# Kernel tuning notes

Measured on AMD Instinct MI355X. Metric: run time of the kernel, lower is better.

Reference implementation:

```python
import jax, jax.numpy as jnp
import numpy as np

D, H, DK, DF = 512, 8, 64, 2048  # dim, heads, head_dim, forward_dim
EPS = 1e-5


def _layernorm(x, g, b):
    mu = jnp.mean(x, axis=-1, keepdims=True)
    var = jnp.mean(jnp.square(x - mu), axis=-1, keepdims=True)
    return (x - mu) * jax.lax.rsqrt(var + EPS) * g + b


def setup_inputs() -> dict:
    key = jax.random.key(0)
    ks = jax.random.split(key, 16)
    B, S = 2, 2048
    s_in = 1.0 / np.sqrt(D)
    s_ff = 1.0 / np.sqrt(DF)
    s_cat = 1.0 / np.sqrt(H * DK)
    return {
        "x": jax.random.normal(ks[0], (B, S, D), jnp.float32),
        # per-head Q/K/V projections stacked over heads: [H, D, DK]
        "Wq": jax.random.uniform(ks[1], (H, D, DK), jnp.float32, -s_in, s_in),
        "bq": jax.random.uniform(ks[2], (H, DK), jnp.float32, -s_in, s_in),
        "Wk": jax.random.uniform(ks[3], (H, D, DK), jnp.float32, -s_in, s_in),
        "bk": jax.random.uniform(ks[4], (H, DK), jnp.float32, -s_in, s_in),
        "Wv": jax.random.uniform(ks[5], (H, D, DK), jnp.float32, -s_in, s_in),
        "bv": jax.random.uniform(ks[6], (H, DK), jnp.float32, -s_in, s_in),
        "Wo": jax.random.uniform(ks[7], (H * DK, D), jnp.float32, -s_cat, s_cat),
        "bo": jax.random.uniform(ks[8], (D,), jnp.float32, -s_cat, s_cat),
        "ln1_g": jnp.ones((D,), jnp.float32),
        "ln1_b": jnp.zeros((D,), jnp.float32),
        "W1": jax.random.uniform(ks[9], (D, DF), jnp.float32, -s_in, s_in),
        "b1": jax.random.uniform(ks[10], (DF,), jnp.float32, -s_in, s_in),
        "W2": jax.random.uniform(ks[11], (DF, D), jnp.float32, -s_ff, s_ff),
        "b2": jax.random.uniform(ks[12], (D,), jnp.float32, -s_ff, s_ff),
        "ln2_g": jnp.ones((D,), jnp.float32),
        "ln2_b": jnp.zeros((D,), jnp.float32),
    }


def reference(x, Wq, bq, Wk, bk, Wv, bv, Wo, bo, ln1_g, ln1_b, W1, b1, W2, b2, ln2_g, ln2_b):
    # Per-head projections, batched over heads: [B,H,S,DK]
    q = jnp.einsum('bsd,hdk->bhsk', x, Wq) + bq[None, :, None, :]
    k = jnp.einsum('bsd,hdk->bhsk', x, Wk) + bk[None, :, None, :]
    v = jnp.einsum('bsd,hdk->bhsk', x, Wv) + bv[None, :, None, :]
    scale = 1.0 / np.sqrt(DK)
    scores = jnp.einsum('bhsk,bhtk->bhst', q, k) * scale  # [B,H,S,S]
    attn = jax.nn.softmax(scores, axis=-1)
    o = jnp.einsum('bhst,bhtk->bhsk', attn, v)  # [B,H,S,DK]
    # concat heads (head order matches torch cat over ModuleList)
    B, _, S, _ = o.shape
    o = o.transpose(0, 2, 1, 3).reshape(B, S, H * DK)
    attn_out = o @ Wo + bo
    # Residual 1 (dropout = identity in eval): LN(x + sublayer(x))
    h = _layernorm(x + attn_out, ln1_g, ln1_b)
    # FeedForward + Residual 2
    ff = jax.nn.relu(h @ W1 + b1) @ W2 + b2
    return _layernorm(h + ff, ln2_g, ln2_b)
```

## Files before the change

### kernel.cpp

```cpp
#include <hip/hip_runtime.h>


#define Dm   512
#define Hh   8
#define DKk  64
#define DFf  2048
#define Bb   2
#define Ss   2048
#define Nn   4096

typedef __attribute__((ext_vector_type(8))) short short8;
typedef __attribute__((ext_vector_type(4))) float f32x4;
typedef __attribute__((ext_vector_type(4))) short short4v;

__device__ inline float bf2f(short s) {
    unsigned u = ((unsigned)(unsigned short)s) << 16;
    float f; __builtin_memcpy(&f, &u, 4); return f;
}
__device__ inline short f2bf(float f) {
    unsigned u; __builtin_memcpy(&u, &f, 4);
    u = (u + 0x7fff + ((u >> 16) & 1)) >> 16;
    return (short)u;
}
__device__ inline short cvt_elem(const void* p, long i, int f32flag) {
    if (f32flag) return f2bf(((const float*)p)[i]);
    return ((const short*)p)[i];
}
__device__ inline void gload_lds16(const short* g, short* l) {
    __builtin_amdgcn_global_load_lds(
        (const __attribute__((address_space(1))) unsigned int*)g,
        (__attribute__((address_space(3))) unsigned int*)l, 16, 0, 0);
}

__global__ __launch_bounds__(256) void detect_kernel(const void* x, int* flag)
{
    __shared__ int cnt;
    if (threadIdx.x == 0) cnt = 0;
    __syncthreads();
    const float* xf = (const float*)x;
    int ok = 0;
    for (int i = threadIdx.x; i < 1024; i += 256) {
        float a = fabsf(xf[i]);
        if (a > 1e-8f && a < 1e4f) ok++;
    }
    atomicAdd(&cnt, ok);
    __syncthreads();
    if (threadIdx.x == 0) *flag = (cnt >= 512) ? 1 : 0;
}

__global__ __launch_bounds__(256) void convert_kernel(
    const int* __restrict__ flag, const void* __restrict__ x, short* __restrict__ xb,
    const void* bq, const void* bk, const void* bv, const void* bo,
    const void* b1, const void* b2, const void* g1, const void* be1,
    const void* g2, const void* be2, short* __restrict__ smalls)
{
    int f = *flag;
    int blk = blockIdx.x;
    if (blk < 512) {
        long base = (long)blk * 4096;
        for (int i = threadIdx.x; i < 4096; i += 256)
            xb[base + i] = cvt_elem(x, base + i, f);
    } else {
        const void* srcs[10] = {bq, bk, bv, bo, b1, b2, g1, be1, g2, be2};
        const int   sz[10]   = {512, 512, 512, 512, 2048, 512, 512, 512, 512, 512};
        int off = 0;
        for (int j = 0; j < 10; ++j) {
            for (int i = threadIdx.x; i < sz[j]; i += 256)
                smalls[off + i] = cvt_elem(srcs[j], i, f);
            off += sz[j];
        }
    }
}

__global__ __launch_bounds__(256) void transpose_kernel(
    const int* __restrict__ flag,
    const void* Wq, const void* Wk, const void* Wv,
    const void* Wo, const void* W1, const void* W2,
    short* __restrict__ WqkvT,
    short* __restrict__ WoT, short* __restrict__ W1T, short* __restrict__ W2T)
{
    __shared__ short tile[64][65];
    int f = *flag;
    int blk = blockIdx.x;
    const void* src; short* dst; long srcoff = 0; long dstoff = 0; int R, C, tr, tc;
    if (blk < 192) {
        int m = blk >> 6; int r = blk & 63; int h = r >> 3; int t = r & 7;
        src = (m == 0) ? Wq : (m == 1) ? Wk : Wv;
        dst = WqkvT + (long)m * 512 * 512;
        srcoff = (long)h * 512 * 64; dstoff = (long)h * 64 * 512;
        R = 512; C = 64; tr = t; tc = 0;
    } else if (blk < 256) {
        int r = blk - 192; src = Wo; dst = WoT; R = 512; C = 512; tr = r >> 3; tc = r & 7;
    } else if (blk < 512) {
        int r = blk - 256; src = W1; dst = W1T; R = 512; C = 2048; tr = r >> 5; tc = r & 31;
    } else {
        int r = blk - 512; src = W2; dst = W2T; R = 2048; C = 512; tr = r >> 3; tc = r & 7;
    }
    int r0 = tr * 64, c0 = tc * 64;
    for (int i = threadIdx.x; i < 4096; i += 256) {
        int rr = i >> 6, cc = i & 63;
        tile[rr][cc] = cvt_elem(src, srcoff + (long)(r0 + rr) * C + c0 + cc, f);
    }
    __syncthreads();
    for (int i = threadIdx.x; i < 4096; i += 256) {
        int cc = i >> 6, rr = i & 63;
        dst[dstoff + (long)(c0 + cc) * R + r0 + rr] = tile[rr][cc];
    }
}

#define MODE_F32       1
#define MODE_RELU_BF16 2
#define MODE_QKV       4

__global__ __launch_bounds__(256) void gemm_kernel(
    const short* __restrict__ A, const short* __restrict__ Bt,
    const short* __restrict__ bias, void* __restrict__ outp,
    void* __restrict__ out2, void* __restrict__ out3,
    int K, int Ncols, int mode, int Ktile)
{
    __shared__ short As[128 * 32];
    __shared__ short Bs[128 * 32];
    const int t    = threadIdx.x;
    const int lane = t & 63;
    const int wave = t >> 6;
    const int quad = lane >> 4;
    const int l15  = lane & 15;
    const int wm = wave >> 1, wn = wave & 1;
    const int row0 = blockIdx.x * 128;
    const int col0 = blockIdx.y * 128;
    const int kbase = blockIdx.z * Ktile;

    const int srow = t >> 2;
    const int sch  = (t & 3) ^ ((t >> 3) & 3);
    const long ga0 = (long)(row0 + srow) * K + sch * 8 + kbase;
    const long ga1 = (long)(row0 + srow + 64) * K + sch * 8 + kbase;
    const long gb0 = (long)(col0 + srow) * K + sch * 8 + kbase;
    const long gb1 = (long)(col0 + srow + 64) * K + sch * 8 + kbase;
    short* la0 = As + t * 8;
    short* la1 = As + (t + 256) * 8;
    short* lb0 = Bs + t * 8;
    short* lb1 = Bs + (t + 256) * 8;

    f32x4 acc[4][4];
#pragma unroll
    for (int i = 0; i < 4; ++i)
#pragma unroll
        for (int j = 0; j < 4; ++j) acc[i][j] = (f32x4){0.f, 0.f, 0.f, 0.f};

    int aoff[4], boff[4];
#pragma unroll
    for (int mt = 0; mt < 4; ++mt) {
        int rowa = wm * 64 + mt * 16 + l15;
        aoff[mt] = rowa * 32 + (quad ^ ((rowa >> 1) & 3)) * 8;
        int rowb = wn * 64 + mt * 16 + l15;
        boff[mt] = rowb * 32 + (quad ^ ((rowb >> 1) & 3)) * 8;
    }

    for (int k0 = 0; k0 < Ktile; k0 += 32) {
        __syncthreads();
        gload_lds16(A  + ga0 + k0, la0);
        gload_lds16(A  + ga1 + k0, la1);
        gload_lds16(Bt + gb0 + k0, lb0);
        gload_lds16(Bt + gb1 + k0, lb1);
        asm volatile("s_waitcnt vmcnt(0)" ::: "memory");
        __syncthreads();
        short8 af[4], bf[4];
#pragma unroll
        for (int mt = 0; mt < 4; ++mt) af[mt] = *(const short8*)(As + aoff[mt]);
#pragma unroll
        for (int nt = 0; nt < 4; ++nt) bf[nt] = *(const short8*)(Bs + boff[nt]);
#pragma unroll
        for (int mt = 0; mt < 4; ++mt)
#pragma unroll
            for (int nt = 0; nt < 4; ++nt)
                acc[mt][nt] = __builtin_amdgcn_mfma_f32_16x16x32_bf16(
                    af[mt], bf[nt], acc[mt][nt], 0, 0, 0);
    }

    const int wrow0 = row0 + wm * 64;
    const int wcol0 = col0 + wn * 64;
    if (mode == MODE_QKV) {
        int m = wcol0 >> 9;
        if (m < 2) {
            short* out = (short*)(m == 0 ? outp : out2);
#pragma unroll
            for (int nt = 0; nt < 4; ++nt) {
                int col = wcol0 + nt * 16 + l15;
                float bb = bf2f(bias[col]);
                int cl = col & 511;
#pragma unroll
                for (int mt = 0; mt < 4; ++mt)
#pragma unroll
                    for (int r = 0; r < 4; ++r) {
                        int row = wrow0 + mt * 16 + quad * 4 + r;
                        out[(long)row * 512 + cl] = f2bf(acc[mt][nt][r] + bb);
                    }
            }
        } else {
            short* out = (short*)out3;
#pragma unroll
            for (int nt = 0; nt < 4; ++nt) {
                int col = wcol0 + nt * 16 + l15;
                float bb = bf2f(bias[col]);
                int cl = col - 1024;
                int h = cl >> 6, kk = cl & 63;
#pragma unroll
                for (int mt = 0; mt < 4; ++mt)
#pragma unroll
                    for (int r = 0; r < 4; ++r) {
                        int row = wrow0 + mt * 16 + quad * 4 + r;
                        int b = row >> 11, s = row & 2047;
                        out[((long)(b * Hh + h) * DKk + kk) * Ss + s] =
                            f2bf(acc[mt][nt][r] + bb);
                    }
            }
        }
    } else if (mode == MODE_F32) {
        float* out = (float*)outp + (long)blockIdx.z * Nn * Ncols;
        int zb = (blockIdx.z == 0);
#pragma unroll
        for (int nt = 0; nt < 4; ++nt) {
            int col = wcol0 + nt * 16 + l15;
            float bb = zb ? bf2f(bias[col]) : 0.f;
#pragma unroll
            for (int mt = 0; mt < 4; ++mt)
#pragma unroll
                for (int r = 0; r < 4; ++r) {
                    int row = wrow0 + mt * 16 + quad * 4 + r;
                    out[(long)row * Ncols + col] = acc[mt][nt][r] + bb;
                }
        }
    } else {
        short* out = (short*)outp;
#pragma unroll
        for (int nt = 0; nt < 4; ++nt) {
            int col = wcol0 + nt * 16 + l15;
            float bb = bf2f(bias[col]);
#pragma unroll
            for (int mt = 0; mt < 4; ++mt)
#pragma unroll
                for (int r = 0; r < 4; ++r) {
                    int row = wrow0 + mt * 16 + quad * 4 + r;
                    out[(long)row * Ncols + col] = f2bf(fmaxf(acc[mt][nt][r] + bb, 0.f));
                }
        }
    }
}

__global__ __launch_bounds__(256) void attn_kernel(
    const short* __restrict__ Q, const short* __restrict__ Kt,
    const short* __restrict__ Vt, float* __restrict__ po, float* __restrict__ ls)
{
    __shared__ __align__(16) short Ks[2][64 * 64];
    __shared__ __align__(16) short Vs[2][64 * 64];
    __shared__ __align__(16) short pbuf[4][32 * 72];
    const int lane = threadIdx.x & 63;
    const int wave = threadIdx.x >> 6;
    const int quad = lane >> 4;
    const int l15  = lane & 15;
    const int qt = blockIdx.x, bh = blockIdx.y, ks = blockIdx.z;
    const int b = bh >> 3, h = bh & 7;
    const int qrow = b * Ss + qt * 128 + wave * 32;

    short8 aq[2][2];
#pragma unroll
    for (int qh = 0; qh < 2; ++qh)
#pragma unroll
        for (int kk = 0; kk < 2; ++kk)
            aq[qh][kk] = *(const short8*)(Q + (long)(qrow + qh * 16 + l15) * Dm
                                          + h * DKk + kk * 32 + quad * 8);

    f32x4 o[2][4];
    float lsum[2][4];
#pragma unroll
    for (int qh = 0; qh < 2; ++qh) {
#pragma unroll
        for (int nt = 0; nt < 4; ++nt) o[qh][nt] = (f32x4){0.f, 0.f, 0.f, 0.f};
#pragma unroll
        for (int r = 0; r < 4; ++r) lsum[qh][r] = 0.f;
    }

    const short* Kg = Kt + (long)b * Ss * Dm + h * DKk;
    const short* Vg = Vt + (long)bh * DKk * Ss;
    short* pb = pbuf[wave];
    const int t00 = ks * 512;

    const int ri = lane >> 3;
    const int ct = (lane & 7) ^ ri;
    const int ldsrow0 = wave * 16;

    auto stage = [&](int buf, int tkv) {
#pragma unroll
        for (int p = 0; p < 2; ++p) {
            int r = ldsrow0 + p * 8 + ri;
            gload_lds16(Kg + (long)(tkv + r) * Dm + ct * 8,
                        &Ks[buf][(ldsrow0 + p * 8) * 64] + lane * 8);
        }
#pragma unroll
        for (int p = 0; p < 2; ++p) {
            int r = ldsrow0 + p * 8 + ri;
            gload_lds16(Vg + (long)r * Ss + tkv + ct * 8,
                        &Vs[buf][(ldsrow0 + p * 8) * 64] + lane * 8);
        }
    };

    stage(0, t00);
    int cur = 0;
    for (int it = 0; it < 8; ++it) {
        asm volatile("s_waitcnt vmcnt(0)" ::: "memory");
        __syncthreads();
        if (it < 7) stage(cur ^ 1, t00 + (it + 1) * 64);

        f32x4 s[2][4];
#pragma unroll
        for (int j = 0; j < 4; ++j) {
            short8 kf0 = *(const short8*)&Ks[cur][(j * 16 + l15) * 64
                                                  + ((quad) ^ (l15 & 7)) * 8];
            short8 kf1 = *(const short8*)&Ks[cur][(j * 16 + l15) * 64
                                                  + ((4 + quad) ^ (l15 & 7)) * 8];
#pragma unroll
            for (int qh = 0; qh < 2; ++qh) {
                f32x4 sj = (f32x4){0.f, 0.f, 0.f, 0.f};
                sj = __builtin_amdgcn_mfma_f32_16x16x32_bf16(aq[qh][0], kf0, sj, 0, 0, 0);
                sj = __builtin_amdgcn_mfma_f32_16x16x32_bf16(aq[qh][1], kf1, sj, 0, 0, 0);
                s[qh][j] = sj;
            }
        }
#pragma unroll
        for (int qh = 0; qh < 2; ++qh)
#pragma unroll
            for (int j = 0; j < 4; ++j)
#pragma unroll
                for (int r = 0; r < 4; ++r) {
                    float p = __expf(fminf(s[qh][j][r] * 0.125f, 20.f));
                    lsum[qh][r] += p;
                    pb[(qh * 16 + quad * 4 + r) * 72 + j * 16 + l15] = f2bf(p);
                }
        asm volatile("s_waitcnt lgkmcnt(0)" ::: "memory");
#pragma unroll
        for (int c = 0; c < 2; ++c) {
            short8 ap[2];
#pragma unroll
            for (int qh = 0; qh < 2; ++qh)
                ap[qh] = *(const short8*)(pb + (qh * 16 + l15) * 72 + c * 32 + quad * 8);
#pragma unroll
            for (int nt = 0; nt < 4; ++nt) {
                short8 vf = *(const short8*)&Vs[cur][(nt * 16 + l15) * 64
                                                     + ((c * 4 + quad) ^ (l15 & 7)) * 8];
#pragma unroll
                for (int qh = 0; qh < 2; ++qh)
                    o[qh][nt] = __builtin_amdgcn_mfma_f32_16x16x32_bf16(
                        ap[qh], vf, o[qh][nt], 0, 0, 0);
            }
        }
        asm volatile("" ::: "memory");
        cur ^= 1;
    }

#pragma unroll
    for (int qh = 0; qh < 2; ++qh)
#pragma unroll
        for (int r = 0; r < 4; ++r) {
            float v = lsum[qh][r];
            v += __shfl_xor(v, 1);
            v += __shfl_xor(v, 2);
            v += __shfl_xor(v, 4);
            v += __shfl_xor(v, 8);
            lsum[qh][r] = v;
        }
    float* pob = po + ((((long)bh * 16 + qt) * 4 + ks) * 128) * 64;
#pragma unroll
    for (int qh = 0; qh < 2; ++qh)
#pragma unroll
        for (int nt = 0; nt < 4; ++nt)
#pragma unroll
            for (int r = 0; r < 4; ++r)
                pob[(wave * 32 + qh * 16 + quad * 4 + r) * 64 + nt * 16 + l15] =
                    o[qh][nt][r];
    if (l15 == 0) {
        long lbase = (((long)bh * 16 + qt) * 4 + ks) * 128 + wave * 32;
#pragma unroll
        for (int qh = 0; qh < 2; ++qh)
#pragma unroll
            for (int r = 0; r < 4; ++r)
                ls[lbase + qh * 16 + quad * 4 + r] = lsum[qh][r];
    }
}

__global__ __launch_bounds__(256) void combine_kernel(
    const float* __restrict__ po, const float* __restrict__ ls,
    short* __restrict__ O)
{
    const int qt = blockIdx.x, bh = blockIdx.y;
    const int b = bh >> 3, h = bh & 7;
    const long base = ((long)bh * 16 + qt) * 4;
    const int tid = threadIdx.x;
    const int qloc = tid >> 4;
    const int dk0 = (tid & 15) * 4;
#pragma unroll
    for (int q0 = 0; q0 < 8; ++q0) {
        int q = q0 * 16 + qloc;
        f32x4 s = (f32x4){0.f, 0.f, 0.f, 0.f};
        float L = 0.f;
#pragma unroll
        for (int ksp = 0; ksp < 4; ++ksp) {
            s += *(const f32x4*)(po + ((base + ksp) * 128 + q) * 64 + dk0);
            L += ls[(base + ksp) * 128 + q];
        }
        float inv = 1.f / L;
        short4v ov;
#pragma unroll
        for (int i = 0; i < 4; ++i) ov[i] = f2bf(s[i] * inv);
        *(short4v*)(O + (long)(b * Ss + qt * 128 + q) * Dm + h * DKk + dk0) = ov;
    }
}

__global__ __launch_bounds__(256) void ln_kernel(
    const float* __restrict__ v0, const float* __restrict__ v1,
    const float* __restrict__ v2, const float* __restrict__ v3,
    const short* __restrict__ res,
    const short* __restrict__ g, const short* __restrict__ bt,
    void* __restrict__ out, const int* __restrict__ flagp)
{
    const int row = blockIdx.x, tid = threadIdx.x;
    const long base = (long)row * Dm;
    const long i0 = base + tid, i1 = base + 256 + tid;
    float x0 = v0[i0] + bf2f(res[i0]);
    float x1 = v0[i1] + bf2f(res[i1]);
    if (v1) { x0 += v1[i0]; x1 += v1[i1]; }
    if (v2) { x0 += v2[i0]; x1 += v2[i1]; }
    if (v3) { x0 += v3[i0]; x1 += v3[i1]; }

    __shared__ float red[8];
    const int wv = tid >> 6, ln = tid & 63;
    float s = x0 + x1;
#pragma unroll
    for (int mk = 1; mk < 64; mk <<= 1) s += __shfl_xor(s, mk);
    if (!ln) red[wv] = s;
    __syncthreads();
    float mean = (red[0] + red[1] + red[2] + red[3]) * (1.f / 512.f);
    float d0 = x0 - mean, d1 = x1 - mean;
    float q = d0 * d0 + d1 * d1;
#pragma unroll
    for (int mk = 1; mk < 64; mk <<= 1) q += __shfl_xor(q, mk);
    if (!ln) red[4 + wv] = q;
    __syncthreads();
    float rs = rsqrtf((red[4] + red[5] + red[6] + red[7]) * (1.f / 512.f) + 1e-5f);
    float y0 = d0 * rs * bf2f(g[tid])       + bf2f(bt[tid]);
    float y1 = d1 * rs * bf2f(g[256 + tid]) + bf2f(bt[256 + tid]);
    int f32out = flagp ? *flagp : 0;
    if (f32out) {
        float* o = (float*)out;
        o[i0] = y0; o[i1] = y1;
    } else {
        short* o = (short*)out;
        o[i0] = f2bf(y0); o[i1] = f2bf(y1);
    }
}

extern "C" void kernel_launch(void* const* d_in, const int* in_sizes, int n_in,
                              void* d_out, int out_size, void* d_ws, size_t ws_size,
                              hipStream_t stream)
{
    (void)in_sizes; (void)n_in; (void)out_size; (void)ws_size;
    const void* x   = d_in[0];
    const void* Wq  = d_in[1];  const void* bq  = d_in[2];
    const void* Wk  = d_in[3];  const void* bk  = d_in[4];
    const void* Wv  = d_in[5];  const void* bv  = d_in[6];
    const void* Wo  = d_in[7];  const void* bo  = d_in[8];
    const void* g1  = d_in[9];  const void* be1 = d_in[10];
    const void* W1  = d_in[11]; const void* b1  = d_in[12];
    const void* W2  = d_in[13]; const void* b2  = d_in[14];
    const void* g2  = d_in[15]; const void* be2 = d_in[16];

    char* ws = (char*)d_ws;
    size_t off = 0;
    auto alloc = [&](size_t bytes) -> void* {
        void* p = ws + off; off += (bytes + 255) & ~(size_t)255; return p;
    };
    short* WqkvT = (short*)alloc((size_t)3 * Dm * Dm * 2);
    short* WoT   = (short*)alloc((size_t)Dm * Dm * 2);
    short* W1T   = (short*)alloc((size_t)DFf * Dm * 2);
    short* W2T   = (short*)alloc((size_t)Dm * DFf * 2);
    short* xb    = (short*)alloc((size_t)Nn * Dm * 2);
    short* sm    = (short*)alloc((size_t)6656 * 2);
    int*   flag  = (int*)  alloc(256);
    char*  regA  = (char*)alloc((size_t)Nn * DFf * 2);
    short* Qb    = (short*)(regA);
    short* Kb    = (short*)(regA + (size_t)Nn * Dm * 2);
    short* Vt    = (short*)(regA + (size_t)Nn * Dm * 4);
    short* Ob    = (short*)(regA + (size_t)Nn * Dm * 6);
    short* u     = (short*)(regA);
    float* wo_p  = (float*)alloc((size_t)2 * Nn * Dm * 4);
    char*  regC  = (char*)alloc((size_t)16 * 16 * 4 * 128 * 64 * 4
                                + (size_t)16 * 16 * 4 * 128 * 4);
    float* po    = (float*)regC;
    float* lsb   = (float*)(regC + (size_t)16 * 16 * 4 * 128 * 64 * 4);
    float* f2p   = (float*)regC;
    short* h_bf  = (short*)alloc((size_t)Nn * Dm * 2);

    detect_kernel<<<1, 256, 0, stream>>>(x, flag);
    convert_kernel<<<513, 256, 0, stream>>>(flag, x, xb, bq, bk, bv, bo,
                                            b1, b2, g1, be1, g2, be2, sm);
    transpose_kernel<<<768, 256, 0, stream>>>(flag, Wq, Wk, Wv, Wo, W1, W2,
                                              WqkvT, WoT, W1T, W2T);
    gemm_kernel<<<dim3(Nn / 128, 1536 / 128, 1), 256, 0, stream>>>(
        xb, WqkvT, sm + 0, Qb, Kb, Vt, Dm, 1536, MODE_QKV, Dm);
    attn_kernel<<<dim3(Ss / 128, Bb * Hh, 4), 256, 0, stream>>>(Qb, Kb, Vt, po, lsb);
    combine_kernel<<<dim3(Ss / 128, Bb * Hh), 256, 0, stream>>>(po, lsb, Ob);
    gemm_kernel<<<dim3(Nn / 128, Dm / 128, 2), 256, 0, stream>>>(
        Ob, WoT, sm + 1536, wo_p, nullptr, nullptr, Dm, Dm, MODE_F32, Dm / 2);
    ln_kernel<<<Nn, 256, 0, stream>>>(wo_p, wo_p + (long)Nn * Dm, nullptr, nullptr,
                                      xb, sm + 4608, sm + 5120, h_bf, nullptr);
    gemm_kernel<<<dim3(Nn / 128, DFf / 128, 1), 256, 0, stream>>>(
        h_bf, W1T, sm + 2048, u, nullptr, nullptr, Dm, DFf, MODE_RELU_BF16, Dm);
    gemm_kernel<<<dim3(Nn / 128, Dm / 128, 4), 256, 0, stream>>>(
        u, W2T, sm + 4096, f2p, nullptr, nullptr, DFf, Dm, MODE_F32, DFf / 4);
    ln_kernel<<<Nn, 256, 0, stream>>>(f2p, f2p + (long)Nn * Dm, f2p + (long)2 * Nn * Dm,
                                      f2p + (long)3 * Nn * Dm,
                                      h_bf, sm + 5632, sm + 6144, d_out, flag);
}
```

Before: 239.3 us.

## Fuse prep kernels, double-buffer GEMM with BK=64, store attention partials in bf16

Merges the detect, convert and transpose kernels into one prep kernel. Each block now recomputes the fp32 check inline from 16 samples instead of reading a flag. The GEMM moves to a K-tile of 64 with double-buffered LDS, prefetching the next tile while MFMAs run on the current one, and uses a new XOR swizzle. Attention split-K partial outputs are written as bf16 rather than fp32, halving that traffic at some precision cost. The inline check on fewer samples is also less robust than the old one.

```diff
diff --git a/kernel.cpp b/kernel.cpp
--- a/kernel.cpp
+++ b/kernel.cpp
@@ -26,41 +26,41 @@
     if (f32flag) return f2bf(((const float*)p)[i]);
     return ((const short*)p)[i];
 }
+__device__ inline int detect_f32(const void* x) {
+    const float* xf = (const float*)x;
+    int ok = 0;
+#pragma unroll
+    for (int i = 0; i < 16; ++i) {
+        float a = fabsf(xf[i]);
+        ok += (a > 1e-8f && a < 1e4f) ? 1 : 0;
+    }
+    return ok >= 8;
+}
 __device__ inline void gload_lds16(const short* g, short* l) {
     __builtin_amdgcn_global_load_lds(
         (const __attribute__((address_space(1))) unsigned int*)g,
         (__attribute__((address_space(3))) unsigned int*)l, 16, 0, 0);
 }
 
-__global__ __launch_bounds__(256) void detect_kernel(const void* x, int* flag)
-{
-    __shared__ int cnt;
-    if (threadIdx.x == 0) cnt = 0;
-    __syncthreads();
-    const float* xf = (const float*)x;
-    int ok = 0;
-    for (int i = threadIdx.x; i < 1024; i += 256) {
-        float a = fabsf(xf[i]);
-        if (a > 1e-8f && a < 1e4f) ok++;
-    }
-    atomicAdd(&cnt, ok);
-    __syncthreads();
-    if (threadIdx.x == 0) *flag = (cnt >= 512) ? 1 : 0;
-}
-
-__global__ __launch_bounds__(256) void convert_kernel(
-    const int* __restrict__ flag, const void* __restrict__ x, short* __restrict__ xb,
+__global__ __launch_bounds__(256) void prep_kernel(
+    const void* __restrict__ x, short* __restrict__ xb,
     const void* bq, const void* bk, const void* bv, const void* bo,
     const void* b1, const void* b2, const void* g1, const void* be1,
-    const void* g2, const void* be2, short* __restrict__ smalls)
+    const void* g2, const void* be2, short* __restrict__ smalls,
+    const void* Wq, const void* Wk, const void* Wv,
+    const void* Wo, const void* W1, const void* W2,
+    short* __restrict__ WqkvT,
+    short* __restrict__ WoT, short* __restrict__ W1T, short* __restrict__ W2T)
 {
-    int f = *flag;
+    const int f = detect_f32(x);
     int blk = blockIdx.x;
     if (blk < 512) {
         long base = (long)blk * 4096;
         for (int i = threadIdx.x; i < 4096; i += 256)
             xb[base + i] = cvt_elem(x, base + i, f);
-    } else {
+        return;
+    }
+    if (blk == 512) {
         const void* srcs[10] = {bq, bk, bv, bo, b1, b2, g1, be1, g2, be2};
         const int   sz[10]   = {512, 512, 512, 512, 2048, 512, 512, 512, 512, 512};
         int off = 0;
@@ -69,19 +69,10 @@
                 smalls[off + i] = cvt_elem(srcs[j], i, f);
             off += sz[j];
         }
-    }
-}
-
-__global__ __launch_bounds__(256) void transpose_kernel(
-    const int* __restrict__ flag,
-    const void* Wq, const void* Wk, const void* Wv,
-    const void* Wo, const void* W1, const void* W2,
-    short* __restrict__ WqkvT,
-    short* __restrict__ WoT, short* __restrict__ W1T, short* __restrict__ W2T)
-{
+        return;
+    }
     __shared__ short tile[64][65];
-    int f = *flag;
-    int blk = blockIdx.x;
+    blk -= 513;
     const void* src; short* dst; long srcoff = 0; long dstoff = 0; int R, C, tr, tc;
     if (blk < 192) {
         int m = blk >> 6; int r = blk & 63; int h = r >> 3; int t = r & 7;
@@ -118,8 +109,8 @@
     void* __restrict__ out2, void* __restrict__ out3,
     int K, int Ncols, int mode, int Ktile)
 {
-    __shared__ short As[128 * 32];
-    __shared__ short Bs[128 * 32];
+    __shared__ short As[2][128 * 64];
+    __shared__ short Bs[2][128 * 64];
     const int t    = threadIdx.x;
     const int lane = t & 63;
     const int wave = t >> 6;
@@ -130,16 +121,8 @@
     const int col0 = blockIdx.y * 128;
     const int kbase = blockIdx.z * Ktile;
 
-    const int srow = t >> 2;
-    const int sch  = (t & 3) ^ ((t >> 3) & 3);
-    const long ga0 = (long)(row0 + srow) * K + sch * 8 + kbase;
-    const long ga1 = (long)(row0 + srow + 64) * K + sch * 8 + kbase;
-    const long gb0 = (long)(col0 + srow) * K + sch * 8 + kbase;
-    const long gb1 = (long)(col0 + srow + 64) * K + sch * 8 + kbase;
-    short* la0 = As + t * 8;
-    short* la1 = As + (t + 256) * 8;
-    short* lb0 = Bs + t * 8;
-    short* lb1 = Bs + (t + 256) * 8;
+    const int ri = lane >> 3;
+    const int ct = (lane & 7) ^ ri;
 
     f32x4 acc[4][4];
 #pragma unroll
@@ -147,34 +130,51 @@
 #pragma unroll
         for (int j = 0; j < 4; ++j) acc[i][j] = (f32x4){0.f, 0.f, 0.f, 0.f};
 
-    int aoff[4], boff[4];
-#pragma unroll
-    for (int mt = 0; mt < 4; ++mt) {
-        int rowa = wm * 64 + mt * 16 + l15;
-        aoff[mt] = rowa * 32 + (quad ^ ((rowa >> 1) & 3)) * 8;
-        int rowb = wn * 64 + mt * 16 + l15;
-        boff[mt] = rowb * 32 + (quad ^ ((rowb >> 1) & 3)) * 8;
-    }
-
-    for (int k0 = 0; k0 < Ktile; k0 += 32) {
-        __syncthreads();
-        gload_lds16(A  + ga0 + k0, la0);
-        gload_lds16(A  + ga1 + k0, la1);
-        gload_lds16(Bt + gb0 + k0, lb0);
-        gload_lds16(Bt + gb1 + k0, lb1);
+    auto stage = [&](int buf, int k0) {
+#pragma unroll
+        for (int p = 0; p < 4; ++p) {
+            int r = wave * 32 + p * 8;
+            gload_lds16(A + (long)(row0 + r + ri) * K + kbase + k0 + ct * 8,
+                        &As[buf][r * 64 + lane * 8]);
+        }
+#pragma unroll
+        for (int p = 0; p < 4; ++p) {
+            int r = wave * 32 + p * 8;
+            gload_lds16(Bt + (long)(col0 + r + ri) * K + kbase + k0 + ct * 8,
+                        &Bs[buf][r * 64 + lane * 8]);
+        }
+    };
+
+    stage(0, 0);
+    int cur = 0;
+    const int niter = Ktile >> 6;
+    for (int it = 0; it < niter; ++it) {
         asm volatile("s_waitcnt vmcnt(0)" ::: "memory");
         __syncthreads();
-        short8 af[4], bf[4];
-#pragma unroll
-        for (int mt = 0; mt < 4; ++mt) af[mt] = *(const short8*)(As + aoff[mt]);
-#pragma unroll
-        for (int nt = 0; nt < 4; ++nt) bf[nt] = *(const short8*)(Bs + boff[nt]);
-#pragma unroll
-        for (int mt = 0; mt < 4; ++mt)
-#pragma unroll
-            for (int nt = 0; nt < 4; ++nt)
-                acc[mt][nt] = __builtin_amdgcn_mfma_f32_16x16x32_bf16(
-                    af[mt], bf[nt], acc[mt][nt], 0, 0, 0);
+        if (it + 1 < niter) stage(cur ^ 1, (it + 1) * 64);
+#pragma unroll
+        for (int kk = 0; kk < 2; ++kk) {
+            short8 af[4], bfr[4];
+#pragma unroll
+            for (int mt = 0; mt < 4; ++mt) {
+                int rowa = wm * 64 + mt * 16 + l15;
+                af[mt] = *(const short8*)&As[cur][rowa * 64
+                              + (((kk * 4 + quad) ^ (rowa & 7)) * 8)];
+            }
+#pragma unroll
+            for (int nt = 0; nt < 4; ++nt) {
+                int rowb = wn * 64 + nt * 16 + l15;
+                bfr[nt] = *(const short8*)&Bs[cur][rowb * 64
+                              + (((kk * 4 + quad) ^ (rowb & 7)) * 8)];
+            }
+#pragma unroll
+            for (int mt = 0; mt < 4; ++mt)
+#pragma unroll
+                for (int nt = 0; nt < 4; ++nt)
+                    acc[mt][nt] = __builtin_amdgcn_mfma_f32_16x16x32_bf16(
+                        af[mt], bfr[nt], acc[mt][nt], 0, 0, 0);
+        }
+        cur ^= 1;
     }
 
     const int wrow0 = row0 + wm * 64;
@@ -249,7 +249,7 @@
 
 __global__ __launch_bounds__(256) void attn_kernel(
     const short* __restrict__ Q, const short* __restrict__ Kt,
-    const short* __restrict__ Vt, float* __restrict__ po, float* __restrict__ ls)
+    const short* __restrict__ Vt, short* __restrict__ po, float* __restrict__ ls)
 {
     __shared__ __align__(16) short Ks[2][64 * 64];
     __shared__ __align__(16) short Vs[2][64 * 64];
@@ -368,7 +368,7 @@
             v += __shfl_xor(v, 8);
             lsum[qh][r] = v;
         }
-    float* pob = po + ((((long)bh * 16 + qt) * 4 + ks) * 128) * 64;
+    short* pob = po + ((((long)bh * 16 + qt) * 4 + ks) * 128) * 64;
 #pragma unroll
     for (int qh = 0; qh < 2; ++qh)
 #pragma unroll
@@ -376,7 +376,7 @@
 #pragma unroll
             for (int r = 0; r < 4; ++r)
                 pob[(wave * 32 + qh * 16 + quad * 4 + r) * 64 + nt * 16 + l15] =
-                    o[qh][nt][r];
+                    f2bf(o[qh][nt][r]);
     if (l15 == 0) {
         long lbase = (((long)bh * 16 + qt) * 4 + ks) * 128 + wave * 32;
 #pragma unroll
@@ -388,7 +388,7 @@
 }
 
 __global__ __launch_bounds__(256) void combine_kernel(
-    const float* __restrict__ po, const float* __restrict__ ls,
+    const short* __restrict__ po, const float* __restrict__ ls,
     short* __restrict__ O)
 {
     const int qt = blockIdx.x, bh = blockIdx.y;
@@ -404,7 +404,9 @@
         float L = 0.f;
 #pragma unroll
         for (int ksp = 0; ksp < 4; ++ksp) {
-            s += *(const f32x4*)(po + ((base + ksp) * 128 + q) * 64 + dk0);
+            short4v pv = *(const short4v*)(po + ((base + ksp) * 128 + q) * 64 + dk0);
+#pragma unroll
+            for (int i = 0; i < 4; ++i) s[i] += bf2f(pv[i]);
             L += ls[(base + ksp) * 128 + q];
         }
         float inv = 1.f / L;
@@ -420,7 +422,7 @@
     const float* __restrict__ v2, const float* __restrict__ v3,
     const short* __restrict__ res,
     const short* __restrict__ g, const short* __restrict__ bt,
-    void* __restrict__ out, const int* __restrict__ flagp)
+    void* __restrict__ out, const void* __restrict__ xdet)
 {
     const int row = blockIdx.x, tid = threadIdx.x;
     const long base = (long)row * Dm;
@@ -448,7 +450,7 @@
     float rs = rsqrtf((red[4] + red[5] + red[6] + red[7]) * (1.f / 512.f) + 1e-5f);
     float y0 = d0 * rs * bf2f(g[tid])       + bf2f(bt[tid]);
     float y1 = d1 * rs * bf2f(g[256 + tid]) + bf2f(bt[256 + tid]);
-    int f32out = flagp ? *flagp : 0;
+    int f32out = xdet ? detect_f32(xdet) : 0;
     if (f32out) {
         float* o = (float*)out;
         o[i0] = y0; o[i1] = y1;
@@ -484,7 +486,6 @@
     short* W2T   = (short*)alloc((size_t)Dm * DFf * 2);
     short* xb    = (short*)alloc((size_t)Nn * Dm * 2);
     short* sm    = (short*)alloc((size_t)6656 * 2);
-    int*   flag  = (int*)  alloc(256);
     char*  regA  = (char*)alloc((size_t)Nn * DFf * 2);
     short* Qb    = (short*)(regA);
     short* Kb    = (short*)(regA + (size_t)Nn * Dm * 2);
@@ -492,18 +493,16 @@
     short* Ob    = (short*)(regA + (size_t)Nn * Dm * 6);
     short* u     = (short*)(regA);
     float* wo_p  = (float*)alloc((size_t)2 * Nn * Dm * 4);
-    char*  regC  = (char*)alloc((size_t)16 * 16 * 4 * 128 * 64 * 4
-                                + (size_t)16 * 16 * 4 * 128 * 4);
-    float* po    = (float*)regC;
-    float* lsb   = (float*)(regC + (size_t)16 * 16 * 4 * 128 * 64 * 4);
+    char*  regC  = (char*)alloc((size_t)4 * Nn * Dm * 4);
+    short* po    = (short*)regC;
     float* f2p   = (float*)regC;
+    float* lsb   = (float*)alloc((size_t)16 * 16 * 4 * 128 * 4);
     short* h_bf  = (short*)alloc((size_t)Nn * Dm * 2);
 
-    detect_kernel<<<1, 256, 0, stream>>>(x, flag);
-    convert_kernel<<<513, 256, 0, stream>>>(flag, x, xb, bq, bk, bv, bo,
-                                            b1, b2, g1, be1, g2, be2, sm);
-    transpose_kernel<<<768, 256, 0, stream>>>(flag, Wq, Wk, Wv, Wo, W1, W2,
-                                              WqkvT, WoT, W1T, W2T);
+    prep_kernel<<<1281, 256, 0, stream>>>(x, xb, bq, bk, bv, bo, b1, b2,
+                                          g1, be1, g2, be2, sm,
+                                          Wq, Wk, Wv, Wo, W1, W2,
+                                          WqkvT, WoT, W1T, W2T);
     gemm_kernel<<<dim3(Nn / 128, 1536 / 128, 1), 256, 0, stream>>>(
         xb, WqkvT, sm + 0, Qb, Kb, Vt, Dm, 1536, MODE_QKV, Dm);
     attn_kernel<<<dim3(Ss / 128, Bb * Hh, 4), 256, 0, stream>>>(Qb, Kb, Vt, po, lsb);
@@ -518,5 +517,5 @@
         u, W2T, sm + 4096, f2p, nullptr, nullptr, DFf, Dm, MODE_F32, DFf / 4);
     ln_kernel<<<Nn, 256, 0, stream>>>(f2p, f2p + (long)Nn * Dm, f2p + (long)2 * Nn * Dm,
                                       f2p + (long)3 * Nn * Dm,
-                                      h_bf, sm + 5632, sm + 6144, d_out, flag);
-}
+                                      h_bf, sm + 5632, sm + 6144, d_out, x);
+}
```

Result: faster. 214.6 us (-10.3%).
